# Performance work log

Measured on AMD Instinct MI355X. Metric: run time of the kernel, lower is better.

The kernel has to match this reference:

```python
import jax, jax.numpy as jnp
import numpy as np

DIM = 2048        # config.dim
HID = 1408        # config.moe_inter_dim
E = 16            # config.n_routed_experts
TOPK = 4          # config.n_activated_experts
SHARED = 2816     # n_shared_experts * moe_inter_dim
B, S = 1, 2048
ROUTE_SCALE = 1.0


def setup_inputs() -> dict:
    key = jax.random.key(0)
    ks = jax.random.split(key, 8)
    def w(k, shape, fan_in):
        return jax.random.normal(k, shape, jnp.float32) * (1.0 / np.sqrt(fan_in))
    return {
        "x": jax.random.normal(ks[0], (B, S, DIM), jnp.float32),
        "gate_w": w(ks[1], (E, DIM), DIM),
        "w1": w(ks[2], (E, HID, DIM), DIM),   # per-expert nn.Linear(dim, hid).weight
        "w2": w(ks[3], (E, DIM, HID), HID),   # per-expert nn.Linear(hid, dim).weight
        "w3": w(ks[4], (E, HID, DIM), DIM),
        "sw1": w(ks[5], (SHARED, DIM), DIM),  # shared MLP weights
        "sw2": w(ks[6], (DIM, SHARED), SHARED),
        "sw3": w(ks[7], (SHARED, DIM), DIM),
    }


def reference(x, gate_w, w1, w2, w3, sw1, sw2, sw3):
    shape = x.shape
    xt = x.reshape(-1, DIM)                      # [T, D]
    T = xt.shape[0]

    # --- Gate (score_func='softmax', n_groups=1, bias=None since dim != 7168) ---
    logits = xt @ gate_w.T                        # [T, E]
    scores = jax.nn.softmax(logits.astype(jnp.float32), axis=-1)
    topv, idx = jax.lax.top_k(scores, TOPK)       # n_groups==1: topk over flat scores
    weights = topv * ROUTE_SCALE                  # gather(original_scores, idx) == topv here

    # aux load-balance loss
    tpe = jnp.zeros((E,), jnp.float32).at[idx.reshape(-1)].add(1.0) / (T * TOPK)
    aux_loss = E * jnp.sum(tpe * scores.mean(axis=0))

    # --- Routed experts: combine weights [T, E], then batched SwiGLU GEMMs ---
    comb = jnp.zeros((T, E), jnp.float32).at[jnp.arange(T)[:, None], idx].add(weights)
    h = jax.nn.silu(jnp.einsum('td,ehd->teh', xt, w1)) * jnp.einsum('td,ehd->teh', xt, w3)
    y = jnp.einsum('teh,edh,te->td', h, w2, comb)  # weighted combine (0-weight experts cancel)

    # --- Shared experts (SwiGLU MLP, dropout=0) ---
    z = (jax.nn.silu(xt @ sw1.T) * (xt @ sw3.T)) @ sw2.T

    return (y + z).reshape(shape), aux_loss
```

## Files before the change

### kernel.cpp

```cpp
#include <hip/hip_runtime.h>
#include <hip/hip_bf16.h>

typedef unsigned short u16;
typedef __attribute__((ext_vector_type(8))) short short8;
typedef __attribute__((ext_vector_type(4))) float f32x4;

#define DIM 2048
#define HID 1408
#define NE 16
#define NTOK 2048
#define TOPK_ 4
#define SHID 2816
#define CAPROWS 10240
#define MAXTILES (CAPROWS / 128)
#define AUX_IDX (2048 * 2048)

__device__ inline u16 f2bf(float f) {
  __bf16 h = (__bf16)f;
  return __builtin_bit_cast(u16, h);
}

__device__ inline void gload_lds16(const void* g, void* l) {
  __builtin_amdgcn_global_load_lds(
      (const __attribute__((address_space(1))) unsigned int*)g,
      (__attribute__((address_space(3))) unsigned int*)l, 16, 0, 0);
}

__global__ __launch_bounds__(256) void gate_dots_kernel(
    const float* __restrict__ x, const float* __restrict__ gw,
    double* __restrict__ logits) {
  int t = blockIdx.x;
  const float* xt = x + (size_t)t * DIM;
  __shared__ double red[NE][4];
  int lane = threadIdx.x & 63, wid = threadIdx.x >> 6;
  for (int e = 0; e < NE; ++e) {
    const float* w = gw + e * DIM;
    double p = 0.0;
    for (int d = threadIdx.x; d < DIM; d += 256)
      p += (double)xt[d] * (double)w[d];
#pragma unroll
    for (int s = 32; s; s >>= 1) p += __shfl_xor(p, s);
    if (lane == 0) red[e][wid] = p;
  }
  __syncthreads();
  if (threadIdx.x < NE) {
    int e = threadIdx.x;
    logits[(size_t)t * NE + e] = red[e][0] + red[e][1] + red[e][2] + red[e][3];
  }
}

__global__ __launch_bounds__(256) void topk_kernel(
    const double* __restrict__ logits,
    int* __restrict__ idxb, float* __restrict__ wtb,
    int* __restrict__ counts, float* __restrict__ ssum) {
  __shared__ int lcnt[NE];
  __shared__ float lsum[NE];
  if (threadIdx.x < NE) { lcnt[threadIdx.x] = 0; lsum[threadIdx.x] = 0.f; }
  __syncthreads();
  int t = blockIdx.x * 256 + threadIdx.x;
  int lane = threadIdx.x & 63;
  double sc[NE];
  double m = -1e300;
#pragma unroll
  for (int e = 0; e < NE; ++e) {
    sc[e] = logits[(size_t)t * NE + e];
    if (sc[e] > m) m = sc[e];
  }
  double s = 0.0;
#pragma unroll
  for (int e = 0; e < NE; ++e) { sc[e] = exp(sc[e] - m); s += sc[e]; }
  double inv = 1.0 / s;
#pragma unroll
  for (int e = 0; e < NE; ++e) sc[e] *= inv;
  unsigned used = 0;
  for (int k = 0; k < TOPK_; ++k) {
    int be = 0; double bv = -1.0;
#pragma unroll
    for (int e = 0; e < NE; ++e)
      if (!((used >> e) & 1u) && sc[e] > bv) { bv = sc[e]; be = e; }
    used |= 1u << be;
    idxb[t * TOPK_ + k] = be;
    wtb[t * TOPK_ + k] = (float)bv;
    atomicAdd(&lcnt[be], 1);
  }
#pragma unroll
  for (int e = 0; e < NE; ++e) {
    float v = (float)sc[e];
#pragma unroll
    for (int sft = 32; sft; sft >>= 1) v += __shfl_xor(v, sft);
    if (lane == 0) atomicAdd(&lsum[e], v);
  }
  __syncthreads();
  if (threadIdx.x < NE) {
    atomicAdd(&counts[threadIdx.x], lcnt[threadIdx.x]);
    atomicAdd(&ssum[threadIdx.x], lsum[threadIdx.x]);
  }
}

__global__ __launch_bounds__(256) void setup_kernel(
    const int* __restrict__ counts, int* __restrict__ off, int* __restrict__ cap,
    const float* __restrict__ ssum, int* __restrict__ perm, float* __restrict__ pwt,
    float* __restrict__ aux_out,
    int* __restrict__ tile2e, int* __restrict__ tile2m0) {
  for (int i = threadIdx.x; i < MAXTILES; i += 256) tile2e[i] = -1;
  __syncthreads();
  if (threadIdx.x == 0) {
    int o = 0; double aux = 0.0; int nt = 0;
    for (int e = 0; e < NE; ++e) {
      off[e] = o;
      int c = (counts[e] + 127) & ~127;
      cap[e] = c;
      for (int t = 0; t < (c >> 7); ++t) {
        int slot = (nt / 10) + (nt % 10) * 8;
        tile2e[slot] = e;
        tile2m0[slot] = o + t * 128;
        ++nt;
      }
      o += c;
      aux += ((double)counts[e] / (NTOK * TOPK_)) * ((double)ssum[e] / NTOK);
    }
    aux_out[0] = (float)(NE * aux);
  }
  for (int i = threadIdx.x; i < CAPROWS; i += 256) { perm[i] = 0; pwt[i] = 0.f; }
}

__global__ __launch_bounds__(256) void scatter_kernel(
    const int* __restrict__ idxb, const float* __restrict__ wtb,
    const int* __restrict__ off, int* __restrict__ cursor,
    int* __restrict__ perm, float* __restrict__ pwt) {
  int t = blockIdx.x * 256 + threadIdx.x;
  if (t >= NTOK) return;
  for (int k = 0; k < TOPK_; ++k) {
    int e = idxb[t * TOPK_ + k];
    int s = atomicAdd(&cursor[e], 1);
    int p = off[e] + s;
    perm[p] = t;
    pwt[p] = wtb[t * TOPK_ + k];
  }
}

__global__ __launch_bounds__(256) void cvtN_kernel(const float* __restrict__ in,
                                                   u16* __restrict__ out, long n) {
  long stride = (long)gridDim.x * 2048;
  for (long i = ((long)blockIdx.x * 256 + threadIdx.x) * 8; i < n; i += stride) {
    float4 a = *(const float4*)(in + i);
    float4 b = *(const float4*)(in + i + 4);
    union { u16 u[8]; uint4 v; } o;
    o.u[0] = f2bf(a.x); o.u[1] = f2bf(a.y); o.u[2] = f2bf(a.z); o.u[3] = f2bf(a.w);
    o.u[4] = f2bf(b.x); o.u[5] = f2bf(b.y); o.u[6] = f2bf(b.z); o.u[7] = f2bf(b.w);
    *(uint4*)(out + i) = o.v;
  }
}

template <bool GATHER, bool DUAL, int EPI>
__global__ __launch_bounds__(256) void gemm7_kernel(
    const u16* __restrict__ A, int lda,
    const float* __restrict__ B1, const float* __restrict__ B3,
    int ldb, long bstride, int K,
    const int* __restrict__ tile2e, const int* __restrict__ tile2m0,
    const int* __restrict__ seg_off, const int* __restrict__ seg_cnt,
    const int* __restrict__ perm, const float* __restrict__ pwt,
    float* __restrict__ C0, int ldc0,
    u16* __restrict__ Cb, int ldcb, int Mfixed) {
  int e, m0, rowlim;
  if (tile2e) {
    e = tile2e[blockIdx.x];
    if (e < 0) return;
    m0 = tile2m0[blockIdx.x];
    rowlim = seg_off[e] + seg_cnt[e];
  } else {
    e = 0;
    m0 = blockIdx.x * 128;
    if (m0 >= Mfixed) return;
    rowlim = Mfixed;
  }
  int n0 = blockIdx.y * 64;
  const float* Bb1 = B1 + (long)e * bstride;
  const float* Bb3 = DUAL ? (B3 + (long)e * bstride) : nullptr;

  __shared__ u16 As[2][128 * 64];
  __shared__ u16 Bs1[2][64 * 64];
  __shared__ u16 Bs3[DUAL ? 2 : 1][DUAL ? 64 * 64 : 1];

  int tid = threadIdx.x;
  int lane = tid & 63;
  int wid = tid >> 6;
  int wr = wid >> 1, wc = wid & 1;

  f32x4 acc1[4][2], acc3[4][2];
#pragma unroll
  for (int mi = 0; mi < 4; ++mi)
#pragma unroll
    for (int ni = 0; ni < 2; ++ni) {
      acc1[mi][ni] = (f32x4){0.f, 0.f, 0.f, 0.f};
      acc3[mi][ni] = (f32x4){0.f, 0.f, 0.f, 0.f};
    }

  int sr = tid >> 3;
  int scA = tid & 7;
  long abase[4];
#pragma unroll
  for (int it = 0; it < 4; ++it) {
    int row = m0 + it * 32 + sr;
    int rid = GATHER ? perm[row] : row;
    abase[it] = (long)rid * lda + ((scA ^ (sr & 7)) << 3);
  }
  int brr = tid >> 4;
  int gB = tid & 15;
  int wofs = (((gB >> 1) ^ (brr & 7)) << 3) + ((gB & 1) << 2);
  long bbase[4];
#pragma unroll
  for (int it = 0; it < 4; ++it)
    bbase[it] = (long)(n0 + it * 16 + brr) * ldb + gB * 4;

  float4 r1[4], r3[4];

  auto stageA = [&](int buf, int k0) {
#pragma unroll
    for (int it = 0; it < 4; ++it)
      gload_lds16(A + abase[it] + k0, &As[buf][(it * 32 + sr) * 64 + scA * 8]);
  };
  auto loadB = [&](int k0) {
#pragma unroll
    for (int it = 0; it < 4; ++it) r1[it] = *(const float4*)(Bb1 + bbase[it] + k0);
    if (DUAL) {
#pragma unroll
      for (int it = 0; it < 4; ++it) r3[it] = *(const float4*)(Bb3 + bbase[it] + k0);
    }
  };
  auto writeB = [&](int buf) {
#pragma unroll
    for (int it = 0; it < 4; ++it) {
      int lo = (it * 16 + brr) * 64 + wofs;
      ushort4 o;
      o.x = f2bf(r1[it].x); o.y = f2bf(r1[it].y); o.z = f2bf(r1[it].z); o.w = f2bf(r1[it].w);
      *(ushort4*)&Bs1[buf][lo] = o;
      if (DUAL) {
        ushort4 q;
        q.x = f2bf(r3[it].x); q.y = f2bf(r3[it].y); q.z = f2bf(r3[it].z); q.w = f2bf(r3[it].w);
        *(ushort4*)&Bs3[buf][lo] = q;
      }
    }
  };

  loadB(0);
  stageA(0, 0);
  int NT = K >> 6;
  int cur = 0;
  for (int t = 0; t < NT; ++t) {
    int nxt = cur ^ 1;
    writeB(cur);
    if (t + 1 < NT) {
      loadB((t + 1) << 6);
      stageA(nxt, (t + 1) << 6);
      if (DUAL) asm volatile("s_waitcnt vmcnt(12)" ::: "memory");
      else      asm volatile("s_waitcnt vmcnt(8)"  ::: "memory");
    } else {
      asm volatile("s_waitcnt vmcnt(0)" ::: "memory");
    }
    asm volatile("s_waitcnt lgkmcnt(0)" ::: "memory");
    __builtin_amdgcn_sched_barrier(0);
    __builtin_amdgcn_s_barrier();
    __builtin_amdgcn_sched_barrier(0);
#pragma unroll
    for (int kk = 0; kk < 64; kk += 32) {
      short8 af[4], b1f[2], b3f[2];
#pragma unroll
      for (int i = 0; i < 4; ++i) {
        int R = wr * 64 + i * 16 + (lane & 15);
        int c = (kk >> 3) + (lane >> 4);
        af[i] = *(const short8*)&As[cur][R * 64 + ((c ^ (R & 7)) << 3)];
      }
#pragma unroll
      for (int i = 0; i < 2; ++i) {
        int r = wc * 32 + i * 16 + (lane & 15);
        int cR = (kk >> 3) + (lane >> 4);
        b1f[i] = *(const short8*)&Bs1[cur][r * 64 + ((cR ^ (r & 7)) << 3)];
        if (DUAL)
          b3f[i] = *(const short8*)&Bs3[cur][r * 64 + ((cR ^ (r & 7)) << 3)];
      }
#pragma unroll
      for (int mi = 0; mi < 4; ++mi)
#pragma unroll
        for (int ni = 0; ni < 2; ++ni) {
          acc1[mi][ni] = __builtin_amdgcn_mfma_f32_16x16x32_bf16(af[mi], b1f[ni], acc1[mi][ni], 0, 0, 0);
          if (DUAL)
            acc3[mi][ni] = __builtin_amdgcn_mfma_f32_16x16x32_bf16(af[mi], b3f[ni], acc3[mi][ni], 0, 0, 0);
        }
    }
    __builtin_amdgcn_sched_barrier(0);
    __builtin_amdgcn_s_barrier();
    cur = nxt;
  }

  int rbase = m0 + wr * 64 + (lane >> 4) * 4;
  int cbase = n0 + wc * 32 + (lane & 15);
#pragma unroll
  for (int mi = 0; mi < 4; ++mi) {
#pragma unroll
    for (int ni = 0; ni < 2; ++ni) {
      int col = cbase + ni * 16;
#pragma unroll
      for (int r = 0; r < 4; ++r) {
        int row = rbase + mi * 16 + r;
        float v = acc1[mi][ni][r];
        if (EPI == 0) {
          float a3 = acc3[mi][ni][r];
          float sg = v / (1.f + __expf(-v));
          Cb[(long)row * ldcb + col] = f2bf(sg * a3);
        } else if (EPI == 1) {
          C0[(long)row * ldc0 + col] = v;
        } else {
          if (row < rowlim) {
            atomicAdd(&C0[(long)perm[row] * ldc0 + col], v * pwt[row]);
          }
        }
      }
    }
  }
}

extern "C" void kernel_launch(void* const* d_in, const int* in_sizes, int n_in,
                              void* d_out, int out_size, void* d_ws, size_t ws_size,
                              hipStream_t stream) {
  (void)in_sizes; (void)n_in; (void)out_size; (void)ws_size;
  const float* x   = (const float*)d_in[0];
  const float* gw  = (const float*)d_in[1];
  const float* w1  = (const float*)d_in[2];
  const float* w2  = (const float*)d_in[3];
  const float* w3  = (const float*)d_in[4];
  const float* sw1 = (const float*)d_in[5];
  const float* sw2 = (const float*)d_in[6];
  const float* sw3 = (const float*)d_in[7];
  float* out = (float*)d_out;
  char* ws = (char*)d_ws;

  int*   counts = (int*)(ws + 0);
  int*   cursor = (int*)(ws + 64);
  int*   off    = (int*)(ws + 128);
  int*   cap    = (int*)(ws + 192);
  float* ssum   = (float*)(ws + 256);
  int*   tile2e = (int*)(ws + 1024);
  int*   tile2m0= (int*)(ws + 2048);
  int*   idxb   = (int*)(ws + 4096);
  float* wtb    = (float*)(ws + 4096 + 32768);
  int*   perm   = (int*)(ws + 4096 + 65536);
  float* pwt    = (float*)(ws + 4096 + 65536 + 40960);
  u16*   xb     = (u16*)(ws + 262144);
  double* logits = (double*)(ws + 8650752);
  u16*   hbuf   = (u16*)(ws + 16777216);
  u16*   hsb    = (u16*)(ws + 45613056);

  hipMemsetAsync(ws, 0, 512, stream);
  gate_dots_kernel<<<dim3(NTOK), dim3(256), 0, stream>>>(x, gw, logits);
  topk_kernel<<<dim3(NTOK / 256), dim3(256), 0, stream>>>(logits, idxb, wtb, counts, ssum);
  setup_kernel<<<dim3(1), dim3(256), 0, stream>>>(counts, off, cap, ssum, perm, pwt,
                                                  out + AUX_IDX, tile2e, tile2m0);
  scatter_kernel<<<dim3(8), dim3(256), 0, stream>>>(idxb, wtb, off, cursor, perm, pwt);
  cvtN_kernel<<<dim3(2048), dim3(256), 0, stream>>>(x, xb, (long)NTOK * DIM);

  gemm7_kernel<true, true, 0><<<dim3(MAXTILES, HID / 64), dim3(256), 0, stream>>>(
      xb, DIM, w1, w3, DIM, (long)HID * DIM, DIM, tile2e, tile2m0,
      off, counts, perm, pwt, nullptr, 0, hbuf, HID, 0);
  gemm7_kernel<false, true, 0><<<dim3(NTOK / 128, SHID / 64), dim3(256), 0, stream>>>(
      xb, DIM, sw1, sw3, DIM, 0, DIM, nullptr, nullptr,
      nullptr, nullptr, nullptr, nullptr, nullptr, 0, hsb, SHID, NTOK);
  gemm7_kernel<false, false, 1><<<dim3(NTOK / 128, DIM / 64), dim3(256), 0, stream>>>(
      hsb, SHID, sw2, nullptr, SHID, 0, SHID, nullptr, nullptr,
      nullptr, nullptr, nullptr, nullptr, out, DIM, nullptr, 0, NTOK);
  gemm7_kernel<false, false, 2><<<dim3(MAXTILES, DIM / 64), dim3(256), 0, stream>>>(
      hbuf, HID, w2, nullptr, HID, (long)DIM * HID, HID, tile2e, tile2m0,
      off, counts, perm, pwt, out, DIM, nullptr, 0, 0);
}
```

Measured before the change: 642.7 us.

## Enlarge GEMM M-tile to 256 rows with K-step 32 and 4x4 warp fragments

Changes the GEMM tiling from 128x64 tiles with a K-step of 64 to 256x64 tiles with a K-step of 32. Each wave now computes a 64x64 sub-tile, which gives more MFMA reuse per B fragment. Expert capacity padding moves to multiples of 256, and the tile count, slot mapping and workspace offsets are resized to match. The aim is to halve the fp32 weight reloads and conversions per output row. The cost is more padding waste in routed experts, fewer blocks, and roughly double the accumulator registers in the dual-B kernel, which may spill or cut occupancy.

New measurement: 990.8 us. 1.54x slower.

```diff
diff --git a/kernel.cpp b/kernel.cpp
--- a/kernel.cpp
+++ b/kernel.cpp
@@ -11,8 +11,8 @@
 #define NTOK 2048
 #define TOPK_ 4
 #define SHID 2816
-#define CAPROWS 10240
-#define MAXTILES (CAPROWS / 128)
+#define CAPROWS 12288
+#define MAXTILES 48
 #define AUX_IDX (2048 * 2048)
 
 __device__ inline u16 f2bf(float f) {
@@ -108,12 +108,12 @@
     int o = 0; double aux = 0.0; int nt = 0;
     for (int e = 0; e < NE; ++e) {
       off[e] = o;
-      int c = (counts[e] + 127) & ~127;
+      int c = (counts[e] + 255) & ~255;
       cap[e] = c;
-      for (int t = 0; t < (c >> 7); ++t) {
-        int slot = (nt / 10) + (nt % 10) * 8;
+      for (int t = 0; t < (c >> 8); ++t) {
+        int slot = (nt / 6) + (nt % 6) * 8;
         tile2e[slot] = e;
-        tile2m0[slot] = o + t * 128;
+        tile2m0[slot] = o + t * 256;
         ++nt;
       }
       o += c;
@@ -153,7 +153,7 @@
 }
 
 template <bool GATHER, bool DUAL, int EPI>
-__global__ __launch_bounds__(256) void gemm7_kernel(
+__global__ __launch_bounds__(256) void gemm8_kernel(
     const u16* __restrict__ A, int lda,
     const float* __restrict__ B1, const float* __restrict__ B3,
     int ldb, long bstride, int K,
@@ -170,7 +170,7 @@
     rowlim = seg_off[e] + seg_cnt[e];
   } else {
     e = 0;
-    m0 = blockIdx.x * 128;
+    m0 = blockIdx.x * 256;
     if (m0 >= Mfixed) return;
     rowlim = Mfixed;
   }
@@ -178,60 +178,59 @@
   const float* Bb1 = B1 + (long)e * bstride;
   const float* Bb3 = DUAL ? (B3 + (long)e * bstride) : nullptr;
 
-  __shared__ u16 As[2][128 * 64];
-  __shared__ u16 Bs1[2][64 * 64];
-  __shared__ u16 Bs3[DUAL ? 2 : 1][DUAL ? 64 * 64 : 1];
+  __shared__ u16 As[2][256 * 32];
+  __shared__ u16 Bs1[2][64 * 32];
+  __shared__ u16 Bs3[DUAL ? 2 : 1][DUAL ? 64 * 32 : 1];
 
   int tid = threadIdx.x;
   int lane = tid & 63;
-  int wid = tid >> 6;
-  int wr = wid >> 1, wc = wid & 1;
-
-  f32x4 acc1[4][2], acc3[4][2];
+  int wr = tid >> 6;
+
+  f32x4 acc1[4][4], acc3[4][4];
 #pragma unroll
   for (int mi = 0; mi < 4; ++mi)
 #pragma unroll
-    for (int ni = 0; ni < 2; ++ni) {
+    for (int ni = 0; ni < 4; ++ni) {
       acc1[mi][ni] = (f32x4){0.f, 0.f, 0.f, 0.f};
       acc3[mi][ni] = (f32x4){0.f, 0.f, 0.f, 0.f};
     }
 
-  int sr = tid >> 3;
-  int scA = tid & 7;
+  int arw = tid >> 2;
+  int ach = tid & 3;
   long abase[4];
 #pragma unroll
   for (int it = 0; it < 4; ++it) {
-    int row = m0 + it * 32 + sr;
+    int row = m0 + it * 64 + arw;
     int rid = GATHER ? perm[row] : row;
-    abase[it] = (long)rid * lda + ((scA ^ (sr & 7)) << 3);
-  }
-  int brr = tid >> 4;
-  int gB = tid & 15;
-  int wofs = (((gB >> 1) ^ (brr & 7)) << 3) + ((gB & 1) << 2);
-  long bbase[4];
-#pragma unroll
-  for (int it = 0; it < 4; ++it)
-    bbase[it] = (long)(n0 + it * 16 + brr) * ldb + gB * 4;
-
-  float4 r1[4], r3[4];
+    abase[it] = (long)rid * lda + ((ach ^ (arw & 3)) << 3);
+  }
+  int brw = tid >> 3;
+  int gB = tid & 7;
+  long bbase[2];
+#pragma unroll
+  for (int it = 0; it < 2; ++it)
+    bbase[it] = (long)(n0 + it * 32 + brw) * ldb + gB * 4;
+  int wofs = (((gB >> 1) ^ (brw & 3)) << 3) + ((gB & 1) << 2);
+
+  float4 r1[2], r3[2];
 
   auto stageA = [&](int buf, int k0) {
 #pragma unroll
     for (int it = 0; it < 4; ++it)
-      gload_lds16(A + abase[it] + k0, &As[buf][(it * 32 + sr) * 64 + scA * 8]);
+      gload_lds16(A + abase[it] + k0, &As[buf][(it * 64 + arw) * 32 + ach * 8]);
   };
   auto loadB = [&](int k0) {
 #pragma unroll
-    for (int it = 0; it < 4; ++it) r1[it] = *(const float4*)(Bb1 + bbase[it] + k0);
+    for (int it = 0; it < 2; ++it) r1[it] = *(const float4*)(Bb1 + bbase[it] + k0);
     if (DUAL) {
 #pragma unroll
-      for (int it = 0; it < 4; ++it) r3[it] = *(const float4*)(Bb3 + bbase[it] + k0);
+      for (int it = 0; it < 2; ++it) r3[it] = *(const float4*)(Bb3 + bbase[it] + k0);
     }
   };
   auto writeB = [&](int buf) {
 #pragma unroll
-    for (int it = 0; it < 4; ++it) {
-      int lo = (it * 16 + brr) * 64 + wofs;
+    for (int it = 0; it < 2; ++it) {
+      int lo = (it * 32 + brw) * 32 + wofs;
       ushort4 o;
       o.x = f2bf(r1[it].x); o.y = f2bf(r1[it].y); o.z = f2bf(r1[it].z); o.w = f2bf(r1[it].w);
       *(ushort4*)&Bs1[buf][lo] = o;
@@ -245,16 +244,16 @@
 
   loadB(0);
   stageA(0, 0);
-  int NT = K >> 6;
+  int NT = K >> 5;
   int cur = 0;
   for (int t = 0; t < NT; ++t) {
     int nxt = cur ^ 1;
     writeB(cur);
     if (t + 1 < NT) {
-      loadB((t + 1) << 6);
-      stageA(nxt, (t + 1) << 6);
-      if (DUAL) asm volatile("s_waitcnt vmcnt(12)" ::: "memory");
-      else      asm volatile("s_waitcnt vmcnt(8)"  ::: "memory");
+      loadB((t + 1) << 5);
+      stageA(nxt, (t + 1) << 5);
+      if (DUAL) asm volatile("s_waitcnt vmcnt(8)" ::: "memory");
+      else      asm volatile("s_waitcnt vmcnt(6)" ::: "memory");
     } else {
       asm volatile("s_waitcnt vmcnt(0)" ::: "memory");
     }
@@ -262,27 +261,25 @@
     __builtin_amdgcn_sched_barrier(0);
     __builtin_amdgcn_s_barrier();
     __builtin_amdgcn_sched_barrier(0);
-#pragma unroll
-    for (int kk = 0; kk < 64; kk += 32) {
-      short8 af[4], b1f[2], b3f[2];
-#pragma unroll
-      for (int i = 0; i < 4; ++i) {
-        int R = wr * 64 + i * 16 + (lane & 15);
-        int c = (kk >> 3) + (lane >> 4);
-        af[i] = *(const short8*)&As[cur][R * 64 + ((c ^ (R & 7)) << 3)];
-      }
-#pragma unroll
-      for (int i = 0; i < 2; ++i) {
-        int r = wc * 32 + i * 16 + (lane & 15);
-        int cR = (kk >> 3) + (lane >> 4);
-        b1f[i] = *(const short8*)&Bs1[cur][r * 64 + ((cR ^ (r & 7)) << 3)];
+    {
+      short8 af[4], b1f[4], b3f[4];
+      int c = lane >> 4;
+#pragma unroll
+      for (int mi = 0; mi < 4; ++mi) {
+        int R = wr * 64 + mi * 16 + (lane & 15);
+        af[mi] = *(const short8*)&As[cur][R * 32 + ((c ^ (R & 3)) << 3)];
+      }
+#pragma unroll
+      for (int ni = 0; ni < 4; ++ni) {
+        int r = ni * 16 + (lane & 15);
+        b1f[ni] = *(const short8*)&Bs1[cur][r * 32 + ((c ^ (r & 3)) << 3)];
         if (DUAL)
-          b3f[i] = *(const short8*)&Bs3[cur][r * 64 + ((cR ^ (r & 7)) << 3)];
+          b3f[ni] = *(const short8*)&Bs3[cur][r * 32 + ((c ^ (r & 3)) << 3)];
       }
 #pragma unroll
       for (int mi = 0; mi < 4; ++mi)
 #pragma unroll
-        for (int ni = 0; ni < 2; ++ni) {
+        for (int ni = 0; ni < 4; ++ni) {
           acc1[mi][ni] = __builtin_amdgcn_mfma_f32_16x16x32_bf16(af[mi], b1f[ni], acc1[mi][ni], 0, 0, 0);
           if (DUAL)
             acc3[mi][ni] = __builtin_amdgcn_mfma_f32_16x16x32_bf16(af[mi], b3f[ni], acc3[mi][ni], 0, 0, 0);
@@ -294,11 +291,11 @@
   }
 
   int rbase = m0 + wr * 64 + (lane >> 4) * 4;
-  int cbase = n0 + wc * 32 + (lane & 15);
+  int cbase = n0 + (lane & 15);
 #pragma unroll
   for (int mi = 0; mi < 4; ++mi) {
 #pragma unroll
-    for (int ni = 0; ni < 2; ++ni) {
+    for (int ni = 0; ni < 4; ++ni) {
       int col = cbase + ni * 16;
 #pragma unroll
       for (int r = 0; r < 4; ++r) {
@@ -343,13 +340,13 @@
   int*   tile2e = (int*)(ws + 1024);
   int*   tile2m0= (int*)(ws + 2048);
   int*   idxb   = (int*)(ws + 4096);
-  float* wtb    = (float*)(ws + 4096 + 32768);
-  int*   perm   = (int*)(ws + 4096 + 65536);
-  float* pwt    = (float*)(ws + 4096 + 65536 + 40960);
+  float* wtb    = (float*)(ws + 40960);
+  int*   perm   = (int*)(ws + 131072);
+  float* pwt    = (float*)(ws + 196608);
   u16*   xb     = (u16*)(ws + 262144);
   double* logits = (double*)(ws + 8650752);
   u16*   hbuf   = (u16*)(ws + 16777216);
-  u16*   hsb    = (u16*)(ws + 45613056);
+  u16*   hsb    = (u16*)(ws + 51380224);
 
   hipMemsetAsync(ws, 0, 512, stream);
   gate_dots_kernel<<<dim3(NTOK), dim3(256), 0, stream>>>(x, gw, logits);
@@ -359,16 +356,16 @@
   scatter_kernel<<<dim3(8), dim3(256), 0, stream>>>(idxb, wtb, off, cursor, perm, pwt);
   cvtN_kernel<<<dim3(2048), dim3(256), 0, stream>>>(x, xb, (long)NTOK * DIM);
 
-  gemm7_kernel<true, true, 0><<<dim3(MAXTILES, HID / 64), dim3(256), 0, stream>>>(
+  gemm8_kernel<true, true, 0><<<dim3(MAXTILES, HID / 64), dim3(256), 0, stream>>>(
       xb, DIM, w1, w3, DIM, (long)HID * DIM, DIM, tile2e, tile2m0,
       off, counts, perm, pwt, nullptr, 0, hbuf, HID, 0);
-  gemm7_kernel<false, true, 0><<<dim3(NTOK / 128, SHID / 64), dim3(256), 0, stream>>>(
+  gemm8_kernel<false, true, 0><<<dim3(NTOK / 256, SHID / 64), dim3(256), 0, stream>>>(
       xb, DIM, sw1, sw3, DIM, 0, DIM, nullptr, nullptr,
       nullptr, nullptr, nullptr, nullptr, nullptr, 0, hsb, SHID, NTOK);
-  gemm7_kernel<false, false, 1><<<dim3(NTOK / 128, DIM / 64), dim3(256), 0, stream>>>(
+  gemm8_kernel<false, false, 1><<<dim3(NTOK / 256, DIM / 64), dim3(256), 0, stream>>>(
       hsb, SHID, sw2, nullptr, SHID, 0, SHID, nullptr, nullptr,
       nullptr, nullptr, nullptr, nullptr, out, DIM, nullptr, 0, NTOK);
-  gemm7_kernel<false, false, 2><<<dim3(MAXTILES, DIM / 64), dim3(256), 0, stream>>>(
+  gemm8_kernel<false, false, 2><<<dim3(MAXTILES, DIM / 64), dim3(256), 0, stream>>>(
       hbuf, HID, w2, nullptr, HID, (long)DIM * HID, HID, tile2e, tile2m0,
       off, counts, perm, pwt, out, DIM, nullptr, 0, 0);
 }
```

## Deepen B prefetch to two stages with register double-buffering in GEMM

Applied to the files above, without the earlier changes.

The GEMM main loop now keeps two sets of register buffers for the fp32 B tiles and issues global loads two K-steps ahead, unrolling the loop by two. B shared memory drops from double to single buffering, with the extra barrier separating writes from reads. The aim is to hide more global-load latency for the fp32 weight streams, which are converted to bf16 on the fly. In exchange, register pressure rises (16 extra float4 for DUAL), which may lower occupancy. The loop assumes NT is even, which holds for K=2048, 2816 and 1408.

New measurement: 604.0 us. 1.06x faster.

```diff
diff --git a/kernel.cpp b/kernel.cpp
--- a/kernel.cpp
+++ b/kernel.cpp
@@ -153,7 +153,7 @@
 }
 
 template <bool GATHER, bool DUAL, int EPI>
-__global__ __launch_bounds__(256) void gemm7_kernel(
+__global__ __launch_bounds__(256) void gemm9_kernel(
     const u16* __restrict__ A, int lda,
     const float* __restrict__ B1, const float* __restrict__ B3,
     int ldb, long bstride, int K,
@@ -179,8 +179,8 @@
   const float* Bb3 = DUAL ? (B3 + (long)e * bstride) : nullptr;
 
   __shared__ u16 As[2][128 * 64];
-  __shared__ u16 Bs1[2][64 * 64];
-  __shared__ u16 Bs3[DUAL ? 2 : 1][DUAL ? 64 * 64 : 1];
+  __shared__ u16 Bs1[64 * 64];
+  __shared__ u16 Bs3[DUAL ? 64 * 64 : 1];
 
   int tid = threadIdx.x;
   int lane = tid & 63;
@@ -213,14 +213,14 @@
   for (int it = 0; it < 4; ++it)
     bbase[it] = (long)(n0 + it * 16 + brr) * ldb + gB * 4;
 
-  float4 r1[4], r3[4];
+  float4 R1a[4], R3a[4], R1b[4], R3b[4];
 
   auto stageA = [&](int buf, int k0) {
 #pragma unroll
     for (int it = 0; it < 4; ++it)
       gload_lds16(A + abase[it] + k0, &As[buf][(it * 32 + sr) * 64 + scA * 8]);
   };
-  auto loadB = [&](int k0) {
+  auto loadB = [&](float4 (&r1)[4], float4 (&r3)[4], int k0) {
 #pragma unroll
     for (int it = 0; it < 4; ++it) r1[it] = *(const float4*)(Bb1 + bbase[it] + k0);
     if (DUAL) {
@@ -228,40 +228,21 @@
       for (int it = 0; it < 4; ++it) r3[it] = *(const float4*)(Bb3 + bbase[it] + k0);
     }
   };
-  auto writeB = [&](int buf) {
+  auto writeB = [&](float4 (&r1)[4], float4 (&r3)[4]) {
 #pragma unroll
     for (int it = 0; it < 4; ++it) {
       int lo = (it * 16 + brr) * 64 + wofs;
       ushort4 o;
       o.x = f2bf(r1[it].x); o.y = f2bf(r1[it].y); o.z = f2bf(r1[it].z); o.w = f2bf(r1[it].w);
-      *(ushort4*)&Bs1[buf][lo] = o;
+      *(ushort4*)&Bs1[lo] = o;
       if (DUAL) {
         ushort4 q;
         q.x = f2bf(r3[it].x); q.y = f2bf(r3[it].y); q.z = f2bf(r3[it].z); q.w = f2bf(r3[it].w);
-        *(ushort4*)&Bs3[buf][lo] = q;
+        *(ushort4*)&Bs3[lo] = q;
       }
     }
   };
-
-  loadB(0);
-  stageA(0, 0);
-  int NT = K >> 6;
-  int cur = 0;
-  for (int t = 0; t < NT; ++t) {
-    int nxt = cur ^ 1;
-    writeB(cur);
-    if (t + 1 < NT) {
-      loadB((t + 1) << 6);
-      stageA(nxt, (t + 1) << 6);
-      if (DUAL) asm volatile("s_waitcnt vmcnt(12)" ::: "memory");
-      else      asm volatile("s_waitcnt vmcnt(8)"  ::: "memory");
-    } else {
-      asm volatile("s_waitcnt vmcnt(0)" ::: "memory");
-    }
-    asm volatile("s_waitcnt lgkmcnt(0)" ::: "memory");
-    __builtin_amdgcn_sched_barrier(0);
-    __builtin_amdgcn_s_barrier();
-    __builtin_amdgcn_sched_barrier(0);
+  auto compute = [&](int cur) {
 #pragma unroll
     for (int kk = 0; kk < 64; kk += 32) {
       short8 af[4], b1f[2], b3f[2];
@@ -275,9 +256,9 @@
       for (int i = 0; i < 2; ++i) {
         int r = wc * 32 + i * 16 + (lane & 15);
         int cR = (kk >> 3) + (lane >> 4);
-        b1f[i] = *(const short8*)&Bs1[cur][r * 64 + ((cR ^ (r & 7)) << 3)];
+        b1f[i] = *(const short8*)&Bs1[r * 64 + ((cR ^ (r & 7)) << 3)];
         if (DUAL)
-          b3f[i] = *(const short8*)&Bs3[cur][r * 64 + ((cR ^ (r & 7)) << 3)];
+          b3f[i] = *(const short8*)&Bs3[r * 64 + ((cR ^ (r & 7)) << 3)];
       }
 #pragma unroll
       for (int mi = 0; mi < 4; ++mi)
@@ -288,10 +269,43 @@
             acc3[mi][ni] = __builtin_amdgcn_mfma_f32_16x16x32_bf16(af[mi], b3f[ni], acc3[mi][ni], 0, 0, 0);
         }
     }
-    __builtin_amdgcn_sched_barrier(0);
-    __builtin_amdgcn_s_barrier();
-    cur = nxt;
-  }
+  };
+
+  int NT = K >> 6;
+  loadB(R1a, R3a, 0);
+  stageA(0, 0);
+  loadB(R1b, R3b, 64);
+
+#define GEMM9_STEP(T, CUR, RB1, RB3)                                          \
+  {                                                                           \
+    int t_ = (T);                                                             \
+    writeB(RB1, RB3);                           \
+    bool hasA = (t_ + 1 < NT), hasB = (t_ + 2 < NT);                          \
+    if (hasA) stageA((CUR) ^ 1, (t_ + 1) << 6);                               \
+    if (hasB) loadB(RB1, RB3, (t_ + 2) << 6);                                 \
+    if (hasB) {                                                               \
+      if (DUAL) asm volatile("s_waitcnt vmcnt(20)" ::: "memory");             \
+      else      asm volatile("s_waitcnt vmcnt(12)" ::: "memory");             \
+    } else if (hasA) {                                                        \
+      if (DUAL) asm volatile("s_waitcnt vmcnt(12)" ::: "memory");             \
+      else      asm volatile("s_waitcnt vmcnt(8)"  ::: "memory");             \
+    } else {                                                                  \
+      asm volatile("s_waitcnt vmcnt(0)" ::: "memory");                        \
+    }                                                                         \
+    asm volatile("s_waitcnt lgkmcnt(0)" ::: "memory");                        \
+    __builtin_amdgcn_sched_barrier(0);                                        \
+    __builtin_amdgcn_s_barrier();                    \
+    __builtin_amdgcn_sched_barrier(0);                                        \
+    compute(CUR);                                                             \
+    __builtin_amdgcn_sched_barrier(0);                                        \
+    __builtin_amdgcn_s_barrier();           \
+  }
+
+  for (int t = 0; t < NT; t += 2) {
+    GEMM9_STEP(t,     0, R1a, R3a);
+    GEMM9_STEP(t + 1, 1, R1b, R3b);
+  }
+#undef GEMM9_STEP
 
   int rbase = m0 + wr * 64 + (lane >> 4) * 4;
   int cbase = n0 + wc * 32 + (lane & 15);
@@ -359,16 +373,16 @@
   scatter_kernel<<<dim3(8), dim3(256), 0, stream>>>(idxb, wtb, off, cursor, perm, pwt);
   cvtN_kernel<<<dim3(2048), dim3(256), 0, stream>>>(x, xb, (long)NTOK * DIM);
 
-  gemm7_kernel<true, true, 0><<<dim3(MAXTILES, HID / 64), dim3(256), 0, stream>>>(
+  gemm9_kernel<true, true, 0><<<dim3(MAXTILES, HID / 64), dim3(256), 0, stream>>>(
       xb, DIM, w1, w3, DIM, (long)HID * DIM, DIM, tile2e, tile2m0,
       off, counts, perm, pwt, nullptr, 0, hbuf, HID, 0);
-  gemm7_kernel<false, true, 0><<<dim3(NTOK / 128, SHID / 64), dim3(256), 0, stream>>>(
+  gemm9_kernel<false, true, 0><<<dim3(NTOK / 128, SHID / 64), dim3(256), 0, stream>>>(
       xb, DIM, sw1, sw3, DIM, 0, DIM, nullptr, nullptr,
       nullptr, nullptr, nullptr, nullptr, nullptr, 0, hsb, SHID, NTOK);
-  gemm7_kernel<false, false, 1><<<dim3(NTOK / 128, DIM / 64), dim3(256), 0, stream>>>(
+  gemm9_kernel<false, false, 1><<<dim3(NTOK / 128, DIM / 64), dim3(256), 0, stream>>>(
       hsb, SHID, sw2, nullptr, SHID, 0, SHID, nullptr, nullptr,
       nullptr, nullptr, nullptr, nullptr, out, DIM, nullptr, 0, NTOK);
-  gemm7_kernel<false, false, 2><<<dim3(MAXTILES, DIM / 64), dim3(256), 0, stream>>>(
+  gemm9_kernel<false, false, 2><<<dim3(MAXTILES, DIM / 64), dim3(256), 0, stream>>>(
       hbuf, HID, w2, nullptr, HID, (long)DIM * HID, HID, tile2e, tile2m0,
       off, counts, perm, pwt, out, DIM, nullptr, 0, 0);
 }
```

## Load B fragments directly to registers, bypassing LDS staging in expert GEMMs

Applied to the files above, without the earlier changes.

Replaces the LDS staging of the fp32 weight operand with per-wave direct global loads into registers, converted to bf16 right before the MFMAs. This removes the B LDS writes and reads and restructures the loop to one barrier per k-tile, with A prefetch issued before compute and B prefetch after. In exchange, waves sharing the same columns load the same B data redundantly, and register usage grows.

After: 1.161 ms. +80.6%, slower.

```diff
diff --git a/kernel.cpp b/kernel.cpp
--- a/kernel.cpp
+++ b/kernel.cpp
@@ -153,7 +153,7 @@
 }
 
 template <bool GATHER, bool DUAL, int EPI>
-__global__ __launch_bounds__(256) void gemm7_kernel(
+__global__ __launch_bounds__(256) void gemm10_kernel(
     const u16* __restrict__ A, int lda,
     const float* __restrict__ B1, const float* __restrict__ B3,
     int ldb, long bstride, int K,
@@ -179,8 +179,6 @@
   const float* Bb3 = DUAL ? (B3 + (long)e * bstride) : nullptr;
 
   __shared__ u16 As[2][128 * 64];
-  __shared__ u16 Bs1[2][64 * 64];
-  __shared__ u16 Bs3[DUAL ? 2 : 1][DUAL ? 64 * 64 : 1];
 
   int tid = threadIdx.x;
   int lane = tid & 63;
@@ -205,15 +203,12 @@
     int rid = GATHER ? perm[row] : row;
     abase[it] = (long)rid * lda + ((scA ^ (sr & 7)) << 3);
   }
-  int brr = tid >> 4;
-  int gB = tid & 15;
-  int wofs = (((gB >> 1) ^ (brr & 7)) << 3) + ((gB & 1) << 2);
-  long bbase[4];
-#pragma unroll
-  for (int it = 0; it < 4; ++it)
-    bbase[it] = (long)(n0 + it * 16 + brr) * ldb + gB * 4;
-
-  float4 r1[4], r3[4];
+  long brow[2];
+#pragma unroll
+  for (int ni = 0; ni < 2; ++ni)
+    brow[ni] = (long)(n0 + wc * 32 + ni * 16 + (lane & 15)) * ldb + ((lane >> 4) << 3);
+
+  f32x4 Br1[2][2][2], Br3[2][2][2];
 
   auto stageA = [&](int buf, int k0) {
 #pragma unroll
@@ -222,48 +217,28 @@
   };
   auto loadB = [&](int k0) {
 #pragma unroll
-    for (int it = 0; it < 4; ++it) r1[it] = *(const float4*)(Bb1 + bbase[it] + k0);
-    if (DUAL) {
-#pragma unroll
-      for (int it = 0; it < 4; ++it) r3[it] = *(const float4*)(Bb3 + bbase[it] + k0);
-    }
+    for (int ni = 0; ni < 2; ++ni)
+#pragma unroll
+      for (int kx = 0; kx < 2; ++kx)
+#pragma unroll
+        for (int h = 0; h < 2; ++h) {
+          Br1[ni][kx][h] = *(const f32x4*)(Bb1 + brow[ni] + k0 + kx * 32 + h * 4);
+          if (DUAL)
+            Br3[ni][kx][h] = *(const f32x4*)(Bb3 + brow[ni] + k0 + kx * 32 + h * 4);
+        }
   };
-  auto writeB = [&](int buf) {
-#pragma unroll
-    for (int it = 0; it < 4; ++it) {
-      int lo = (it * 16 + brr) * 64 + wofs;
-      ushort4 o;
-      o.x = f2bf(r1[it].x); o.y = f2bf(r1[it].y); o.z = f2bf(r1[it].z); o.w = f2bf(r1[it].w);
-      *(ushort4*)&Bs1[buf][lo] = o;
-      if (DUAL) {
-        ushort4 q;
-        q.x = f2bf(r3[it].x); q.y = f2bf(r3[it].y); q.z = f2bf(r3[it].z); q.w = f2bf(r3[it].w);
-        *(ushort4*)&Bs3[buf][lo] = q;
-      }
-    }
+  auto cvt8 = [&](const f32x4& lo, const f32x4& hi) {
+    short8 f;
+    f[0] = (short)f2bf(lo[0]); f[1] = (short)f2bf(lo[1]);
+    f[2] = (short)f2bf(lo[2]); f[3] = (short)f2bf(lo[3]);
+    f[4] = (short)f2bf(hi[0]); f[5] = (short)f2bf(hi[1]);
+    f[6] = (short)f2bf(hi[2]); f[7] = (short)f2bf(hi[3]);
+    return f;
   };
-
-  loadB(0);
-  stageA(0, 0);
-  int NT = K >> 6;
-  int cur = 0;
-  for (int t = 0; t < NT; ++t) {
-    int nxt = cur ^ 1;
-    writeB(cur);
-    if (t + 1 < NT) {
-      loadB((t + 1) << 6);
-      stageA(nxt, (t + 1) << 6);
-      if (DUAL) asm volatile("s_waitcnt vmcnt(12)" ::: "memory");
-      else      asm volatile("s_waitcnt vmcnt(8)"  ::: "memory");
-    } else {
-      asm volatile("s_waitcnt vmcnt(0)" ::: "memory");
-    }
-    asm volatile("s_waitcnt lgkmcnt(0)" ::: "memory");
-    __builtin_amdgcn_sched_barrier(0);
-    __builtin_amdgcn_s_barrier();
-    __builtin_amdgcn_sched_barrier(0);
-#pragma unroll
-    for (int kk = 0; kk < 64; kk += 32) {
+  auto compute = [&](int cur) {
+#pragma unroll
+    for (int kx = 0; kx < 2; ++kx) {
+      int kk = kx * 32;
       short8 af[4], b1f[2], b3f[2];
 #pragma unroll
       for (int i = 0; i < 4; ++i) {
@@ -272,12 +247,9 @@
         af[i] = *(const short8*)&As[cur][R * 64 + ((c ^ (R & 7)) << 3)];
       }
 #pragma unroll
-      for (int i = 0; i < 2; ++i) {
-        int r = wc * 32 + i * 16 + (lane & 15);
-        int cR = (kk >> 3) + (lane >> 4);
-        b1f[i] = *(const short8*)&Bs1[cur][r * 64 + ((cR ^ (r & 7)) << 3)];
-        if (DUAL)
-          b3f[i] = *(const short8*)&Bs3[cur][r * 64 + ((cR ^ (r & 7)) << 3)];
+      for (int ni = 0; ni < 2; ++ni) {
+        b1f[ni] = cvt8(Br1[ni][kx][0], Br1[ni][kx][1]);
+        if (DUAL) b3f[ni] = cvt8(Br3[ni][kx][0], Br3[ni][kx][1]);
       }
 #pragma unroll
       for (int mi = 0; mi < 4; ++mi)
@@ -288,8 +260,30 @@
             acc3[mi][ni] = __builtin_amdgcn_mfma_f32_16x16x32_bf16(af[mi], b3f[ni], acc3[mi][ni], 0, 0, 0);
         }
     }
-    __builtin_amdgcn_sched_barrier(0);
-    __builtin_amdgcn_s_barrier();
+  };
+
+  loadB(0);
+  stageA(0, 0);
+  asm volatile("s_waitcnt vmcnt(0)" ::: "memory");
+  __builtin_amdgcn_sched_barrier(0);
+  __builtin_amdgcn_s_barrier();
+  __builtin_amdgcn_sched_barrier(0);
+
+  int NT = K >> 6;
+  int cur = 0;
+  for (int t = 0; t < NT; ++t) {
+    int nxt = cur ^ 1;
+    bool pf = (t + 1 < NT);
+    if (pf) stageA(nxt, (t + 1) << 6);
+    compute(cur);
+    if (pf) {
+      loadB((t + 1) << 6);
+      __builtin_amdgcn_sched_barrier(0);
+      asm volatile("s_waitcnt vmcnt(16)" ::: "memory");
+      __builtin_amdgcn_sched_barrier(0);
+      __builtin_amdgcn_s_barrier();
+      __builtin_amdgcn_sched_barrier(0);
+    }
     cur = nxt;
   }
 
@@ -359,16 +353,16 @@
   scatter_kernel<<<dim3(8), dim3(256), 0, stream>>>(idxb, wtb, off, cursor, perm, pwt);
   cvtN_kernel<<<dim3(2048), dim3(256), 0, stream>>>(x, xb, (long)NTOK * DIM);
 
-  gemm7_kernel<true, true, 0><<<dim3(MAXTILES, HID / 64), dim3(256), 0, stream>>>(
+  gemm10_kernel<true, true, 0><<<dim3(MAXTILES, HID / 64), dim3(256), 0, stream>>>(
       xb, DIM, w1, w3, DIM, (long)HID * DIM, DIM, tile2e, tile2m0,
       off, counts, perm, pwt, nullptr, 0, hbuf, HID, 0);
-  gemm7_kernel<false, true, 0><<<dim3(NTOK / 128, SHID / 64), dim3(256), 0, stream>>>(
+  gemm10_kernel<false, true, 0><<<dim3(NTOK / 128, SHID / 64), dim3(256), 0, stream>>>(
       xb, DIM, sw1, sw3, DIM, 0, DIM, nullptr, nullptr,
       nullptr, nullptr, nullptr, nullptr, nullptr, 0, hsb, SHID, NTOK);
-  gemm7_kernel<false, false, 1><<<dim3(NTOK / 128, DIM / 64), dim3(256), 0, stream>>>(
+  gemm10_kernel<false, false, 1><<<dim3(NTOK / 128, DIM / 64), dim3(256), 0, stream>>>(
       hsb, SHID, sw2, nullptr, SHID, 0, SHID, nullptr, nullptr,
       nullptr, nullptr, nullptr, nullptr, out, DIM, nullptr, 0, NTOK);
-  gemm7_kernel<false, false, 2><<<dim3(MAXTILES, DIM / 64), dim3(256), 0, stream>>>(
+  gemm10_kernel<false, false, 2><<<dim3(MAXTILES, DIM / 64), dim3(256), 0, stream>>>(
       hbuf, HID, w2, nullptr, HID, (long)DIM * HID, HID, tile2e, tile2m0,
       off, counts, perm, pwt, out, DIM, nullptr, 0, 0);
 }
```
